# Performance work log

Hardware: AMD Instinct MI355X
Metric: run time of the kernel (lower is better)

## Reference

```python
import jax, jax.numpy as jnp
import numpy as np

N, E_DIM, T = 32, 512, 2048
N_E = 8192
BETA = 0.25

def setup_inputs() -> dict:
    key = jax.random.key(0)
    k1, k2 = jax.random.split(key)
    z = jax.random.normal(k1, (N, E_DIM, T), dtype=jnp.float32)
    # nn.Embedding weight initialized uniform(-1/n_e, 1/n_e)
    emb = jax.random.uniform(k2, (N_E, E_DIM), dtype=jnp.float32,
                             minval=-1.0 / N_E, maxval=1.0 / N_E)
    return {"z": z, "emb": emb}

def reference(z, emb):
    n, width, t = z.shape
    # preprocess: (N, C, T) -> (N, T, C) -> (N*T, C)
    zf = jnp.transpose(z, (0, 2, 1)).reshape(-1, width)  # [M, e_dim]
    # squared euclidean distances: ||z||^2 + ||e||^2 - 2 z e^T
    d = (jnp.sum(zf ** 2, axis=1, keepdims=True)
         + jnp.sum(emb ** 2, axis=1)
         - 2.0 * jnp.matmul(zf, emb.T))  # [M, n_e]
    idx = jnp.argmin(d, axis=1)  # [M]
    z_q = emb[idx]  # [M, e_dim]
    sg = jax.lax.stop_gradient
    loss = jnp.mean((z_q - sg(zf)) ** 2) + BETA * jnp.mean((sg(z_q) - zf) ** 2)
    # straight-through estimator
    z_q = zf + sg(z_q - zf)
    # (N*T, C) -> (N, T, C) -> (N, C, T)
    z_q = jnp.transpose(z_q.reshape(n, t, width), (0, 2, 1))
    # perplexity from codebook usage histogram
    one_hot = jax.nn.one_hot(idx, emb.shape[0], dtype=zf.dtype)  # [M, n_e]
    e_mean = jnp.mean(one_hot, axis=0)
    perplexity = jnp.exp(-jnp.sum(e_mean * jnp.log(e_mean + 1e-10)))
    return (z_q, loss, perplexity)
```

## Files before the change

kernel.cpp:

```cpp
#include <hip/hip_runtime.h>
#include <stdint.h>

#define NE 8192
#define KD 512
#define MT 65536

typedef __attribute__((ext_vector_type(8))) short bf16x8;
typedef __attribute__((ext_vector_type(4))) float f32x4;

union U128 { uint4 u; bf16x8 b; };

#define WS_SUMZ2   0
#define WS_SUMSMIN 4
#define WS_HIST    8
#define WS_ZEROSZ  40960
#define WS_E2      40960
#define WS_IDX     73728
#define WS_EMB16   335872
#define WS_Z16     8724480

__device__ __forceinline__ unsigned int f2bf(float f) {
    union { float f; unsigned int u; } c; c.f = f;
    return (c.u + 0x7FFFu + ((c.u >> 16) & 1u)) >> 16;
}

__device__ __forceinline__ void load_lds16(const void* g, void* l) {
    __builtin_amdgcn_global_load_lds((const __attribute__((address_space(1))) void*)g,
                                     (__attribute__((address_space(3))) void*)l,
                                     16, 0, 0);
}

__global__ void k_embprep(const float* __restrict__ emb,
                          unsigned short* __restrict__ emb16,
                          float* __restrict__ e2) {
    const int code = blockIdx.x;
    const int lane = threadIdx.x;
    const float4* row = (const float4*)(emb + (size_t)code * KD);
    float4 a = row[lane * 2];
    float4 b = row[lane * 2 + 1];
    float s = a.x*a.x + a.y*a.y + a.z*a.z + a.w*a.w
            + b.x*b.x + b.y*b.y + b.z*b.z + b.w*b.w;
    uint4 o;
    o.x = f2bf(a.x) | (f2bf(a.y) << 16);
    o.y = f2bf(a.z) | (f2bf(a.w) << 16);
    o.z = f2bf(b.x) | (f2bf(b.y) << 16);
    o.w = f2bf(b.z) | (f2bf(b.w) << 16);
    ((uint4*)(emb16 + (size_t)code * KD))[lane] = o;
    #pragma unroll
    for (int off = 32; off; off >>= 1) s += __shfl_down(s, off, 64);
    if (lane == 0) e2[code] = s;
}

__global__ void k_zprep(const float* __restrict__ z,
                        unsigned short* __restrict__ z16,
                        float* __restrict__ sumz2) {
    const int tx = threadIdx.x & 63;
    const int cu = threadIdx.x >> 6;
    const int n  = blockIdx.z;
    const int c0 = blockIdx.y * 32 + cu * 8;
    const int t  = blockIdx.x * 64 + tx;
    const float* base = z + ((size_t)n * KD) * 2048 + t;
    float v[8]; float s = 0.f;
    #pragma unroll
    for (int u = 0; u < 8; u++) {
        v[u] = base[(size_t)(c0 + u) * 2048];
        s += v[u] * v[u];
    }
    uint4 o;
    o.x = f2bf(v[0]) | (f2bf(v[1]) << 16);
    o.y = f2bf(v[2]) | (f2bf(v[3]) << 16);
    o.z = f2bf(v[4]) | (f2bf(v[5]) << 16);
    o.w = f2bf(v[6]) | (f2bf(v[7]) << 16);
    *(uint4*)(z16 + ((size_t)(n * 2048 + t)) * KD + c0) = o;

    #pragma unroll
    for (int off = 32; off; off >>= 1) s += __shfl_down(s, off, 64);
    __shared__ float red[4];
    if ((threadIdx.x & 63) == 0) red[threadIdx.x >> 6] = s;
    __syncthreads();
    if (threadIdx.x == 0) atomicAdd(sumz2, red[0] + red[1] + red[2] + red[3]);
}

__global__ __launch_bounds__(512, 2) void k_main(
    const unsigned short* __restrict__ z16,
    const unsigned short* __restrict__ emb16,
    const float* __restrict__ e2,
    int* __restrict__ g_idx,
    int* __restrict__ hist,
    float* __restrict__ sums)
{
    __shared__ __align__(16) unsigned short zt[128 * 512];
    __shared__ __align__(16) unsigned short et[2][256 * 32];

    const int tid  = threadIdx.x;
    const int lane = tid & 63;
    const int w    = tid >> 6;
    const int wm   = w & 1;
    const int wn   = w >> 1;
    const int quad = lane >> 4;
    const int col  = lane & 15;
    const int m0   = blockIdx.x * 128;

    {
        const int r  = tid >> 2;
        const int jb = (tid & 3) << 4;
        const uint4* gz = (const uint4*)(z16 + (size_t)(m0 + r) * KD);
        uint4* zt4w = (uint4*)zt;
        #pragma unroll
        for (int jj = 0; jj < 16; jj++) {
            int j  = jb + jj;
            int js = (j & 56) | ((j ^ r) & 7);
            zt4w[r * 64 + js] = gz[j];
        }
    }

    const int st_nl0 = w * 16 + (lane >> 2);
    const int st_q8  = (lane & 3) * 8;
    unsigned short* st_l0 = &et[0][0] + w * 512 + lane * 8;
    unsigned short* st_l1 = &et[0][0] + 4096 + w * 512 + lane * 8;

    f32x4 acc[4][4];
    #pragma unroll
    for (int mf = 0; mf < 4; mf++)
        #pragma unroll
        for (int nf = 0; nf < 4; nf++)
            acc[mf][nf] = (f32x4){0.f, 0.f, 0.f, 0.f};

    float rbv[4][4]; int rbi[4][4];
    #pragma unroll
    for (int mf = 0; mf < 4; mf++)
        #pragma unroll
        for (int rg = 0; rg < 4; rg++) { rbv[mf][rg] = 3.0e38f; rbi[mf][rg] = 0; }

    int zbase[4], r7[4];
    #pragma unroll
    for (int mf = 0; mf < 4; mf++) {
        int r = wm * 64 + mf * 16 + col;
        zbase[mf] = r * 64;
        r7[mf] = r & 7;
    }
    int bidx[4];
    #pragma unroll
    for (int nf = 0; nf < 4; nf++)
        bidx[nf] = (wn * 64 + nf * 16 + col) * 4 + quad;

    const uint4* zt4 = (const uint4*)zt;
    const uint4* et4[2] = { (const uint4*)&et[0][0], (const uint4*)&et[1][0] };

    {
        const unsigned short* g0 = emb16 + ((size_t)(st_nl0) << 9) + st_q8;
        const unsigned short* g1 = emb16 + ((size_t)(128 + st_nl0) << 9) + st_q8;
        load_lds16(g0, st_l0);
        load_lds16(g1, st_l1);
    }

    #pragma unroll 1
    for (int chunk = 0; chunk < 32; chunk++) {
        #pragma unroll
        for (int kk = 0; kk < 16; kk++) {
            __syncthreads();
            const int nxt = chunk * 16 + kk + 1;
            if (nxt < 512) {
                const int nchunk = nxt >> 4, nkk = nxt & 15, nbuf = nxt & 1;
                const size_t koff = (size_t)nkk * 32 + st_q8;
                const unsigned short* g0 = emb16 + (((size_t)(nchunk * 256 + st_nl0)) << 9) + koff;
                const unsigned short* g1 = emb16 + (((size_t)(nchunk * 256 + 128 + st_nl0)) << 9) + koff;
                load_lds16(g0, st_l0 + nbuf * 8192);
                load_lds16(g1, st_l1 + nbuf * 8192);
            }
            const int buf = kk & 1;
            const int jhi  = (kk * 4) & 56;
            const int jlow = ((kk & 1) << 2) | quad;
            bf16x8 af[4], bfv[4];
            #pragma unroll
            for (int mf = 0; mf < 4; mf++) {
                U128 u; u.u = zt4[zbase[mf] + (jhi | (jlow ^ r7[mf]))];
                af[mf] = u.b;
            }
            #pragma unroll
            for (int nf = 0; nf < 4; nf++) {
                U128 u; u.u = et4[buf][bidx[nf]];
                bfv[nf] = u.b;
            }
            #pragma unroll
            for (int mf = 0; mf < 4; mf++)
                #pragma unroll
                for (int nf = 0; nf < 4; nf++)
                    acc[mf][nf] = __builtin_amdgcn_mfma_f32_16x16x32_bf16(
                        af[mf], bfv[nf], acc[mf][nf], 0, 0, 0);
        }
        const int nb = chunk * 256 + wn * 64 + col;
        float e2v[4];
        #pragma unroll
        for (int nf = 0; nf < 4; nf++) e2v[nf] = e2[nb + nf * 16];
        #pragma unroll
        for (int mf = 0; mf < 4; mf++) {
            #pragma unroll
            for (int rg = 0; rg < 4; rg++) {
                float v0 = fmaf(-2.f, acc[mf][0][rg], e2v[0]);
                float v1 = fmaf(-2.f, acc[mf][1][rg], e2v[1]);
                float v2 = fmaf(-2.f, acc[mf][2][rg], e2v[2]);
                float v3 = fmaf(-2.f, acc[mf][3][rg], e2v[3]);
                float bv = v0; int bn = 0;
                if (v1 < bv) { bv = v1; bn = 1; }
                if (v2 < bv) { bv = v2; bn = 2; }
                if (v3 < bv) { bv = v3; bn = 3; }
                if (bv < rbv[mf][rg]) { rbv[mf][rg] = bv; rbi[mf][rg] = nb + (bn << 4); }
            }
            #pragma unroll
            for (int nf = 0; nf < 4; nf++)
                acc[mf][nf] = (f32x4){0.f, 0.f, 0.f, 0.f};
        }
    }

    #pragma unroll
    for (int mf = 0; mf < 4; mf++) {
        #pragma unroll
        for (int rg = 0; rg < 4; rg++) {
            float bv = rbv[mf][rg]; int bi = rbi[mf][rg];
            #pragma unroll
            for (int off = 1; off < 16; off <<= 1) {
                float ov = __shfl_xor(bv, off, 64);
                int   oi = __shfl_xor(bi, off, 64);
                if (ov < bv || (ov == bv && oi < bi)) { bv = ov; bi = oi; }
            }
            rbv[mf][rg] = bv; rbi[mf][rg] = bi;
        }
    }

    __syncthreads();
    float* sv = (float*)&et[0][0];
    int*   si = (int*)(sv + 512);
    if (col == 0) {
        #pragma unroll
        for (int mf = 0; mf < 4; mf++)
            #pragma unroll
            for (int rg = 0; rg < 4; rg++) {
                int rl = wm * 64 + mf * 16 + quad * 4 + rg;
                sv[wn * 128 + rl] = rbv[mf][rg];
                si[wn * 128 + rl] = rbi[mf][rg];
            }
    }
    __syncthreads();
    float myv = 0.f;
    if (tid < 128) {
        float bv = sv[tid]; int bi = si[tid];
        #pragma unroll
        for (int wnn = 1; wnn < 4; wnn++) {
            float ov = sv[wnn * 128 + tid]; int oi = si[wnn * 128 + tid];
            if (ov < bv || (ov == bv && oi < bi)) { bv = ov; bi = oi; }
        }
        g_idx[m0 + tid] = bi;
        atomicAdd(&hist[bi], 1);
        myv = bv;
    }
    #pragma unroll
    for (int off = 32; off; off >>= 1) myv += __shfl_down(myv, off, 64);
    if (lane == 0 && w < 2) atomicAdd(&sums[1], myv);
}

__global__ void k_final(const int* __restrict__ hist,
                        const float* __restrict__ sums,
                        float* __restrict__ out_scalars) {
    __shared__ float red[4];
    const int tid = threadIdx.x;
    float s = 0.f;
    for (int i = tid; i < NE; i += 256) {
        float e = (float)hist[i] * (1.0f / 65536.0f);
        s += e * logf(e + 1e-10f);
    }
    #pragma unroll
    for (int off = 32; off; off >>= 1) s += __shfl_down(s, off, 64);
    if ((tid & 63) == 0) red[tid >> 6] = s;
    __syncthreads();
    if (tid == 0) {
        float total = red[0] + red[1] + red[2] + red[3];
        float perp = expf(-total);
        float loss = 1.25f * (sums[0] + sums[1]) / (65536.0f * 512.0f);
        out_scalars[0] = loss;
        out_scalars[1] = perp;
    }
}

__global__ void k_gather(const float* __restrict__ emb,
                         const int* __restrict__ idx,
                         float* __restrict__ out) {
    __shared__ int ids[256];
    const int n  = blockIdx.y;
    const int t0 = blockIdx.x * 256;
    const int tid = threadIdx.x;
    ids[tid] = idx[n * 2048 + t0 + tid];
    __syncthreads();
    const int tq = tid & 63;
    const int cg = tid >> 6;
    const int i0 = ids[tq * 4 + 0];
    const int i1 = ids[tq * 4 + 1];
    const int i2 = ids[tq * 4 + 2];
    const int i3 = ids[tq * 4 + 3];
    const float* e0 = emb + (size_t)i0 * KD;
    const float* e1 = emb + (size_t)i1 * KD;
    const float* e2p = emb + (size_t)i2 * KD;
    const float* e3 = emb + (size_t)i3 * KD;
    for (int c = cg; c < KD; c += 4) {
        float4 o;
        o.x = e0[c]; o.y = e1[c]; o.z = e2p[c]; o.w = e3[c];
        *(float4*)(out + ((size_t)(n * KD + c)) * 2048 + t0 + tq * 4) = o;
    }
}

extern "C" void kernel_launch(void* const* d_in, const int* in_sizes, int n_in,
                              void* d_out, int out_size, void* d_ws, size_t ws_size,
                              hipStream_t stream) {
    (void)in_sizes; (void)n_in; (void)out_size; (void)ws_size;
    const float* z   = (const float*)d_in[0];
    const float* emb = (const float*)d_in[1];
    float* out = (float*)d_out;
    char* ws = (char*)d_ws;

    float*          sums  = (float*)(ws + WS_SUMZ2);
    int*            hist  = (int*)(ws + WS_HIST);
    float*          e2    = (float*)(ws + WS_E2);
    int*            g_idx = (int*)(ws + WS_IDX);
    unsigned short* emb16 = (unsigned short*)(ws + WS_EMB16);
    unsigned short* z16   = (unsigned short*)(ws + WS_Z16);

    hipMemsetAsync(ws, 0, WS_ZEROSZ, stream);

    k_embprep<<<NE, 64, 0, stream>>>(emb, emb16, e2);
    k_zprep<<<dim3(32, 16, 32), 256, 0, stream>>>(z, z16, sums);
    k_main<<<512, 512, 0, stream>>>(z16, emb16, e2, g_idx, hist, sums);
    k_final<<<1, 256, 0, stream>>>(hist, sums, out + 33554432);
    k_gather<<<dim3(8, 32), 256, 0, stream>>>(emb, g_idx, out);
}
```

Measured before the change: 1.074 ms.

## Transpose z via LDS, swizzle embedding tile, vectorize gather loads

k_zprep now stages a 64x64 fp32 tile in padded shared memory, so global reads are coalesced along t and bf16 writes are 16-byte chunks along channels. The embedding stage in k_main rotates the quad offset per row pair to reduce LDS bank conflicts on B-fragment reads, with matching index math on the read side. k_gather loads float4 from each embedding row and writes four channel rows per iteration instead of scalar loads. These changes target memory-bound prep and gather kernels plus LDS conflicts in the main GEMM, at the cost of extra shared memory and index arithmetic.

```diff
diff --git a/kernel.cpp b/kernel.cpp
--- a/kernel.cpp
+++ b/kernel.cpp
@@ -54,31 +54,44 @@
 __global__ void k_zprep(const float* __restrict__ z,
                         unsigned short* __restrict__ z16,
                         float* __restrict__ sumz2) {
-    const int tx = threadIdx.x & 63;
-    const int cu = threadIdx.x >> 6;
+    __shared__ float arr[64][65];
+    __shared__ float red[4];
+    const int tid = threadIdx.x;
     const int n  = blockIdx.z;
-    const int c0 = blockIdx.y * 32 + cu * 8;
-    const int t  = blockIdx.x * 64 + tx;
-    const float* base = z + ((size_t)n * KD) * 2048 + t;
-    float v[8]; float s = 0.f;
-    #pragma unroll
-    for (int u = 0; u < 8; u++) {
-        v[u] = base[(size_t)(c0 + u) * 2048];
-        s += v[u] * v[u];
-    }
-    uint4 o;
-    o.x = f2bf(v[0]) | (f2bf(v[1]) << 16);
-    o.y = f2bf(v[2]) | (f2bf(v[3]) << 16);
-    o.z = f2bf(v[4]) | (f2bf(v[5]) << 16);
-    o.w = f2bf(v[6]) | (f2bf(v[7]) << 16);
-    *(uint4*)(z16 + ((size_t)(n * 2048 + t)) * KD + c0) = o;
-
+    const int c0 = blockIdx.y * 64;
+    const int t0 = blockIdx.x * 64;
+    const int tl = tid & 63;
+    const int cw = tid >> 6;
+    const float* base = z + ((size_t)n * KD + c0) * 2048 + t0;
+    float s = 0.f;
+    #pragma unroll
+    for (int u = 0; u < 16; u++) {
+        int c = u * 4 + cw;
+        float v = base[(size_t)c * 2048 + tl];
+        arr[c][tl] = v;
+        s += v * v;
+    }
     #pragma unroll
     for (int off = 32; off; off >>= 1) s += __shfl_down(s, off, 64);
-    __shared__ float red[4];
-    if ((threadIdx.x & 63) == 0) red[threadIdx.x >> 6] = s;
-    __syncthreads();
-    if (threadIdx.x == 0) atomicAdd(sumz2, red[0] + red[1] + red[2] + red[3]);
+    if (tl == 0) red[cw] = s;
+    __syncthreads();
+    if (tid == 0) atomicAdd(sumz2, red[0] + red[1] + red[2] + red[3]);
+    #pragma unroll
+    for (int iter = 0; iter < 2; iter++) {
+        int task = iter * 256 + tid;
+        int row = task >> 3;
+        int ch  = task & 7;
+        float f0 = arr[ch*8+0][row], f1 = arr[ch*8+1][row],
+              f2v = arr[ch*8+2][row], f3 = arr[ch*8+3][row],
+              f4 = arr[ch*8+4][row], f5 = arr[ch*8+5][row],
+              f6 = arr[ch*8+6][row], f7 = arr[ch*8+7][row];
+        uint4 o;
+        o.x = f2bf(f0) | (f2bf(f1) << 16);
+        o.y = f2bf(f2v) | (f2bf(f3) << 16);
+        o.z = f2bf(f4) | (f2bf(f5) << 16);
+        o.w = f2bf(f6) | (f2bf(f7) << 16);
+        *(uint4*)(z16 + ((size_t)(n * 2048 + t0 + row)) * KD + c0 + ch * 8) = o;
+    }
 }
 
 __global__ __launch_bounds__(512, 2) void k_main(
@@ -115,7 +128,8 @@
     }
 
     const int st_nl0 = w * 16 + (lane >> 2);
-    const int st_q8  = (lane & 3) * 8;
+    const int st_q   = ((lane & 3) - ((st_nl0 >> 1) & 3)) & 3;
+    const int st_q8  = st_q * 8;
     unsigned short* st_l0 = &et[0][0] + w * 512 + lane * 8;
     unsigned short* st_l1 = &et[0][0] + 4096 + w * 512 + lane * 8;
 
@@ -141,8 +155,10 @@
     }
     int bidx[4];
     #pragma unroll
-    for (int nf = 0; nf < 4; nf++)
-        bidx[nf] = (wn * 64 + nf * 16 + col) * 4 + quad;
+    for (int nf = 0; nf < 4; nf++) {
+        int nn = wn * 64 + nf * 16 + col;
+        bidx[nf] = nn * 4 + ((quad + (nn >> 1)) & 3);
+    }
 
     const uint4* zt4 = (const uint4*)zt;
     const uint4* et4[2] = { (const uint4*)&et[0][0], (const uint4*)&et[1][0] };
@@ -293,18 +309,24 @@
     __syncthreads();
     const int tq = tid & 63;
     const int cg = tid >> 6;
-    const int i0 = ids[tq * 4 + 0];
-    const int i1 = ids[tq * 4 + 1];
-    const int i2 = ids[tq * 4 + 2];
-    const int i3 = ids[tq * 4 + 3];
-    const float* e0 = emb + (size_t)i0 * KD;
-    const float* e1 = emb + (size_t)i1 * KD;
-    const float* e2p = emb + (size_t)i2 * KD;
-    const float* e3 = emb + (size_t)i3 * KD;
-    for (int c = cg; c < KD; c += 4) {
-        float4 o;
-        o.x = e0[c]; o.y = e1[c]; o.z = e2p[c]; o.w = e3[c];
-        *(float4*)(out + ((size_t)(n * KD + c)) * 2048 + t0 + tq * 4) = o;
+    const float* e0 = emb + (size_t)ids[tq * 4 + 0] * KD;
+    const float* e1 = emb + (size_t)ids[tq * 4 + 1] * KD;
+    const float* e2p = emb + (size_t)ids[tq * 4 + 2] * KD;
+    const float* e3 = emb + (size_t)ids[tq * 4 + 3] * KD;
+    for (int cb = cg * 4; cb < KD; cb += 16) {
+        float4 a = *(const float4*)(e0 + cb);
+        float4 b = *(const float4*)(e1 + cb);
+        float4 c = *(const float4*)(e2p + cb);
+        float4 d = *(const float4*)(e3 + cb);
+        float* op = out + ((size_t)(n * KD + cb)) * 2048 + t0 + tq * 4;
+        float4 o0 = {a.x, b.x, c.x, d.x};
+        float4 o1 = {a.y, b.y, c.y, d.y};
+        float4 o2 = {a.z, b.z, c.z, d.z};
+        float4 o3 = {a.w, b.w, c.w, d.w};
+        *(float4*)(op)        = o0;
+        *(float4*)(op + 2048) = o1;
+        *(float4*)(op + 4096) = o2;
+        *(float4*)(op + 6144) = o3;
     }
 }
 
@@ -327,7 +349,7 @@
     hipMemsetAsync(ws, 0, WS_ZEROSZ, stream);
 
     k_embprep<<<NE, 64, 0, stream>>>(emb, emb16, e2);
-    k_zprep<<<dim3(32, 16, 32), 256, 0, stream>>>(z, z16, sums);
+    k_zprep<<<dim3(32, 8, 32), 256, 0, stream>>>(z, z16, sums);
     k_main<<<512, 512, 0, stream>>>(z16, emb16, e2, g_idx, hist, sums);
     k_final<<<1, 256, 0, stream>>>(hist, sums, out + 33554432);
     k_gather<<<dim3(8, 32), 256, 0, stream>>>(emb, g_idx, out);
```

New measurement: 918.5 us. 1.17x faster.
